# Optimization experiments

Measured on AMD Instinct MI355X. Metric: run time of the kernel, lower is better.

## Reference

```python
import jax, jax.numpy as jnp
import numpy as np

B = 2048
U_DIM = 128
N_USER = 500000
N_NEWS = 50000
N_WORD = 279215
TITLE_LEN = 10
W_EMB = 50
U_NB = 30   # user_neighbor
N_NB = 30   # news_neighbor
NCAPS = 8
NHID = 16
DIM = NCAPS * NHID          # 128
CNN_OUT = 128
ROUTIT = 4
CONV_CH, KH, KW = 8, 2, 20
PH, PW = 2, 1
FLAT = CONV_CH * ((TITLE_LEN - KH + 1) // PH) * (W_EMB - KW + 1)  # 8*4*31 = 992


def setup_inputs() -> dict:
    key = jax.random.key(0)
    ks = jax.random.split(key, 18)
    nrm = lambda k, s: jax.random.normal(k, s, jnp.float32) * 0.1
    return {
        "user_indices": jax.random.randint(ks[0], (B,), 0, N_USER),
        "news_indices": jax.random.randint(ks[1], (B,), 0, N_NEWS),
        "labels": (jax.random.uniform(ks[2], (B,)) > 0.5).astype(jnp.float32),
        # int neighbor / title tables (module buffers)
        "news_user": jax.random.randint(ks[3], (N_NEWS + 1, U_NB), 0, N_USER),
        "user_news": jax.random.randint(ks[4], (N_USER + 1, N_NB), 0, N_NEWS),
        "title": jax.random.randint(ks[5], (N_NEWS + 1, TITLE_LEN), 0, N_WORD),
        # float parameters
        "user_emb_matrix": nrm(ks[6], (N_USER + 1, U_DIM)),
        "word_emb_matrix": nrm(ks[7], (N_WORD + 1, W_EMB)),
        "conv_w": nrm(ks[8], (CONV_CH, 1, KH, KW)),
        "conv_b": jnp.zeros((CONV_CH,), jnp.float32),
        "dense_w": nrm(ks[9], (FLAT, CNN_OUT)),
        "dense_b": jnp.zeros((CNN_OUT,), jnp.float32),
        "user_weights": nrm(ks[10], (U_DIM, DIM)),
        "user_bias": nrm(ks[11], (DIM,)),
        "item_weights": nrm(ks[12], (CNN_OUT, DIM)),
        "item_bias": nrm(ks[13], (DIM,)),
        "last_w": nrm(ks[14], (DIM, DIM)),
        "last_b": jnp.zeros((DIM,), jnp.float32),
    }


def _convolution(news_ids, title, word_emb, conv_w, conv_b, dense_w, dense_b):
    """Title-CNN news encoder. news_ids: [B, K] int -> [B*K, CNN_OUT]."""
    bk = news_ids.shape[0] * news_ids.shape[1]
    words = title[news_ids.reshape(-1)]              # [BK, L] gather
    x = word_emb[words][:, None, :, :]               # [BK, 1, L, 50]
    y = jax.lax.conv_general_dilated(
        x, conv_w, (1, 1), 'VALID', dimension_numbers=('NCHW', 'OIHW', 'NCHW'))
    y = jax.nn.relu(y + conv_b[None, :, None, None])
    y = jax.lax.reduce_window(y, -jnp.inf, jax.lax.max,
                              (1, 1, PH, PW), (1, 1, PH, PW), 'VALID')
    return jax.nn.relu(y.reshape(bk, -1) @ dense_w + dense_b)


def _routing(x_self, z_nb):
    """Capsule neighbor routing. x_self: [B, DIM], z_nb: [B, K, DIM]."""
    l2n = lambda v: v / (jnp.linalg.norm(v, axis=-1, keepdims=True) + 1e-9)
    x = l2n(x_self.reshape(-1, NCAPS, NHID))
    z = l2n(z_nb.reshape(z_nb.shape[0], z_nb.shape[1], NCAPS, NHID))
    u = x
    for _ in range(ROUTIT):
        p = jax.nn.softmax(jnp.einsum('bkcd,bcd->bkc', z, u), axis=-1)  # over caps
        u = l2n(x + jnp.einsum('bkc,bkcd->bcd', p, z))
    return u.reshape(-1, DIM)


def reference(user_indices, news_indices, labels, news_user, user_news, title,
              user_emb_matrix, word_emb_matrix, conv_w, conv_b, dense_w, dense_b,
              user_weights, user_bias, item_weights, item_bias, last_w, last_b):
    # hop-0 (seed) vectors
    news_v0 = jax.nn.relu(
        _convolution(news_indices[:, None], title, word_emb_matrix,
                     conv_w, conv_b, dense_w, dense_b) @ item_weights + item_bias)  # [B, DIM]
    user_v0 = jax.nn.relu(user_emb_matrix[user_indices] @ user_weights + user_bias)  # [B, DIM]
    # hop-1 neighbor gathers
    news_nb = news_user[news_indices]   # [B, U_NB] user ids clicked this news
    user_nb = user_news[user_indices]   # [B, N_NB] news ids clicked by user
    news_v1 = jax.nn.relu(user_emb_matrix[news_nb] @ user_weights + user_bias)  # [B, U_NB, DIM]
    user_v1 = jax.nn.relu(
        _convolution(user_nb, title, word_emb_matrix, conv_w, conv_b,
                     dense_w, dense_b) @ item_weights + item_bias
    ).reshape(B, N_NB, DIM)
    # capsule routing aggregation
    news_emb = _routing(news_v0, news_v1)
    user_emb = _routing(user_v0, user_v1)
    # simple_dot_net scoring
    x_map = user_emb @ last_w + last_b
    y_map = news_emb @ last_w + last_b
    scores = jnp.sum(x_map * y_map, axis=-1)
    return jax.nn.sigmoid(scores)
```

## Files before the change

kernel.cpp:

```cpp
#include <hip/hip_runtime.h>
#include <hip/hip_bf16.h>
#include <math.h>

#define BSZ 2048
#define NNEWS 50000
#define U_NB 30
#define N_NB 30
#define TITLE_LEN 10
#define W_EMB 50
#define DIM 128
#define ROUTIT 4
#define FLAT2 1024
#define NJOBS (BSZ * 31)

typedef __attribute__((ext_vector_type(8))) short bf16x8;
typedef __attribute__((ext_vector_type(4))) float f32x4;

__device__ __forceinline__ ushort bfbits(float v) {
  __hip_bfloat16 h = __float2bfloat16(v);
  ushort u;
  __builtin_memcpy(&u, &h, 2);
  return u;
}

__device__ __forceinline__ bf16x8 bfrag(const ushort* row, int s) {
  const char* p = reinterpret_cast<const char*>(row) + ((s * 2) & ~15);
  const uint4 lo = *reinterpret_cast<const uint4*>(p);
  const uint4 hi = *reinterpret_cast<const uint4*>(p + 16);
  const uint d0 = lo.x, d1 = lo.y, d2 = lo.z, d3 = lo.w;
  const uint d4 = hi.x, d5 = hi.y, d6 = hi.z, d7 = hi.w;
  const bool q2 = (s & 4) != 0;
  const uint e0 = q2 ? d2 : d0, e1 = q2 ? d3 : d1, e2 = q2 ? d4 : d2;
  const uint e3 = q2 ? d5 : d3, e4 = q2 ? d6 : d4, e5 = q2 ? d7 : d5;
  const bool q1 = (s & 2) != 0;
  const uint f0 = q1 ? e1 : e0, f1 = q1 ? e2 : e1, f2 = q1 ? e3 : e2;
  const uint f3 = q1 ? e4 : e3, f4 = q1 ? e5 : e4;
  const bool r1 = (s & 1) != 0;
  uint g[4];
  g[0] = r1 ? ((f0 >> 16) | (f1 << 16)) : f0;
  g[1] = r1 ? ((f1 >> 16) | (f2 << 16)) : f1;
  g[2] = r1 ? ((f2 >> 16) | (f3 << 16)) : f2;
  g[3] = r1 ? ((f3 >> 16) | (f4 << 16)) : f3;
  bf16x8 r;
  __builtin_memcpy(&r, g, 16);
  return r;
}

__global__ __launch_bounds__(256) void k_prep(
    const float* __restrict__ dw, const float* __restrict__ iw,
    const float* __restrict__ uw, __hip_bfloat16* __restrict__ dwt,
    __hip_bfloat16* __restrict__ iwt, __hip_bfloat16* __restrict__ uwt) {
  const int idx = blockIdx.x * 256 + threadIdx.x;
  if (idx < DIM * FLAT2) {
    const int col = idx & 127, k2 = idx >> 7;
    const int i = k2 & 3, X = k2 >> 2;
    const int c = X & 7, gkq = (X >> 3) & 3, jhq = (X >> 5) & 1, h = X >> 6;
    const int j = jhq * 16 + gkq * 4 + i;
    const float v = (j < 31) ? dw[(c * 124 + h * 31 + j) * 128 + col] : 0.f;
    dwt[col * FLAT2 + k2] = __float2bfloat16(v);
  } else if (idx < DIM * FLAT2 + DIM * DIM) {
    const int j = idx - DIM * FLAT2;
    const int o = j & 127, k = j >> 7;
    iwt[o * DIM + k] = __float2bfloat16(iw[j]);
  } else if (idx < DIM * FLAT2 + 2 * DIM * DIM) {
    const int j = idx - DIM * FLAT2 - DIM * DIM;
    const int o = j & 127, k = j >> 7;
    uwt[o * DIM + k] = __float2bfloat16(uw[j]);
  }
}

__global__ __launch_bounds__(256, 4) void k_conv(
    const int* __restrict__ title, const float* __restrict__ word_emb,
    const float* __restrict__ conv_w, const float* __restrict__ conv_b,
    __hip_bfloat16* __restrict__ flat) {
  __shared__ int s_words[80];
  __shared__ __align__(16) ushort s_x[80 * 64];

  const int tid = threadIdx.x;
  const int wv = tid >> 6, lane = tid & 63;
  const int base = blockIdx.x * 8;
  const int c = lane & 15, gk = lane >> 4;

  bf16x8 b0, b1;
#pragma unroll
  for (int i = 0; i < 8; ++i) {
    const int k = gk * 8 + i;
    float v0 = 0.f, v1 = 0.f;
    if (c < 8 && k < 20) {
      v0 = conv_w[c * 40 + k];
      v1 = conv_w[c * 40 + 20 + k];
    }
    b0[i] = (short)bfbits(v0);
    b1[i] = (short)bfbits(v1);
  }
  const float cbias = (c < 8) ? conv_b[c] : 0.f;

  if (tid < 80) s_words[tid] = title[base * TITLE_LEN + tid];
  __syncthreads();

  {
    const float2* we2 = reinterpret_cast<const float2*>(word_emb);
#pragma unroll
    for (int i = 0; i < 3; ++i) {
      const int u = tid + i * 256;
      if (u < 640) {
        const int row = u >> 3, slot = u & 7;
        ushort o[8];
#pragma unroll
        for (int p = 0; p < 4; ++p) {
          const int c2 = slot * 4 + p;
          float2 v = make_float2(0.f, 0.f);
          if (c2 < 25) v = we2[(long long)s_words[row] * 25 + c2];
          o[2 * p] = bfbits(v.x);
          o[2 * p + 1] = bfbits(v.y);
        }
        *reinterpret_cast<uint4*>(&s_x[row * 64 + slot * 8]) =
            *reinterpret_cast<const uint4*>(o);
      }
    }
  }
  __syncthreads();

  ushort* fl = reinterpret_cast<ushort*>(flat);
#pragma unroll 1
  for (int tt = 0; tt < 2; ++tt) {
    const int t = wv * 2 + tt;
    const ushort* xb = &s_x[t * 640];
    ushort* gout = &fl[(size_t)(base + t) * FLAT2];
#pragma unroll
    for (int jh = 0; jh < 2; ++jh) {
      const int s = jh * 16 + (lane & 15) + gk * 8;
      bf16x8 fprev = bfrag(xb, s);
#pragma unroll
      for (int h = 0; h < 4; ++h) {
        const bf16x8 fmid = bfrag(xb + (2 * h + 1) * 64, s);
        const bf16x8 fnext = bfrag(xb + (2 * h + 2) * 64, s);
        f32x4 d0 = (f32x4){0.f, 0.f, 0.f, 0.f};
        f32x4 d1 = (f32x4){0.f, 0.f, 0.f, 0.f};
        d0 = __builtin_amdgcn_mfma_f32_16x16x32_bf16(fprev, b0, d0, 0, 0, 0);
        d0 = __builtin_amdgcn_mfma_f32_16x16x32_bf16(fmid, b1, d0, 0, 0, 0);
        d1 = __builtin_amdgcn_mfma_f32_16x16x32_bf16(fmid, b0, d1, 0, 0, 0);
        d1 = __builtin_amdgcn_mfma_f32_16x16x32_bf16(fnext, b1, d1, 0, 0, 0);
        if (c < 8) {
          ushort w[4];
#pragma unroll
          for (int i2 = 0; i2 < 4; ++i2)
            w[i2] = bfbits(fmaxf(fmaxf(d0[i2], d1[i2]) + cbias, 0.f));
          *reinterpret_cast<uint2*>(&gout[(h * 64 + jh * 32 + gk * 8 + c) * 4]) =
              *reinterpret_cast<const uint2*>(w);
        }
        fprev = fnext;
      }
    }
  }
}

__global__ __launch_bounds__(256, 2) void k_dense(
    const __hip_bfloat16* __restrict__ flat,
    const __hip_bfloat16* __restrict__ dwt, const float* __restrict__ dense_b,
    const __hip_bfloat16* __restrict__ iwt, const float* __restrict__ item_b,
    __hip_bfloat16* __restrict__ out, int nrows) {
  __shared__ __align__(16) char lds[18432];
  ushort* A0 = (ushort*)lds;
  ushort* A1 = (ushort*)(lds + 9216);
  ushort* c1 = (ushort*)lds;

  const int tid = threadIdx.x;
  const int wv = tid >> 6, lane = tid & 63;
  const int fr = lane & 15, gk = lane >> 4;
  const int lrow0 = min((int)blockIdx.x * 64, nrows - 64);
  const ushort* fl = (const ushort*)flat;
  const ushort* dwp = (const ushort*)dwt;

  uint4 pA[2];
#define LD_A(KS)                                                              \
  {                                                                           \
    _Pragma("unroll") for (int q = 0; q < 2; ++q) {                           \
      const int uu = tid + q * 256;                                           \
      pA[q] = *reinterpret_cast<const uint4*>(                                \
          &fl[(size_t)(lrow0 + (uu >> 3)) * FLAT2 + (KS) * 64 + (uu & 7) * 8]); \
    }                                                                         \
  }
#define ST_A(BUF)                                                             \
  {                                                                           \
    _Pragma("unroll") for (int q = 0; q < 2; ++q) {                           \
      const int uu = tid + q * 256;                                           \
      *reinterpret_cast<uint4*>(&(BUF)[(uu >> 3) * 72 + (uu & 7) * 8]) = pA[q]; \
    }                                                                         \
  }
#define LD_B(DST, KS)                                                         \
  {                                                                           \
    _Pragma("unroll") for (int nn = 0; nn < 2; ++nn)                          \
        _Pragma("unroll") for (int qq = 0; qq < 2; ++qq) {                    \
      (DST)[nn * 2 + qq] = *reinterpret_cast<const bf16x8*>(                  \
          &dwp[(wv * 32 + nn * 16 + fr) * FLAT2 + (KS) * 64 + qq * 32 +       \
               gk * 8]);                                                      \
    }                                                                         \
  }

  LD_A(0);
  ST_A(A0);
  LD_A(1);
  bf16x8 bA[4];
  LD_B(bA, 0);
  __syncthreads();

  f32x4 acc[4][2];
#pragma unroll
  for (int m = 0; m < 4; ++m)
#pragma unroll
    for (int n = 0; n < 2; ++n) acc[m][n] = (f32x4){0.f, 0.f, 0.f, 0.f};

  for (int ks = 0; ks < 16; ++ks) {
    const ushort* cA = (ks & 1) ? A1 : A0;
    bf16x8 bN[4];
    if (ks < 15) {
      LD_B(bN, ks + 1);
    } else {
#pragma unroll
      for (int z = 0; z < 4; ++z) bN[z] = bA[z];
    }
    bf16x8 af[2][4];
#pragma unroll
    for (int kk = 0; kk < 2; ++kk)
#pragma unroll
      for (int m = 0; m < 4; ++m)
        af[kk][m] = *reinterpret_cast<const bf16x8*>(
            &cA[(m * 16 + fr) * 72 + kk * 32 + gk * 8]);
#pragma unroll
    for (int kk = 0; kk < 2; ++kk)
#pragma unroll
      for (int m = 0; m < 4; ++m)
#pragma unroll
        for (int n = 0; n < 2; ++n)
          acc[m][n] = __builtin_amdgcn_mfma_f32_16x16x32_bf16(
              af[kk][m], bA[n * 2 + kk], acc[m][n], 0, 0, 0);
    if (ks < 15) {
      if (ks & 1) {
        ST_A(A0);
      } else {
        ST_A(A1);
      }
    }
    if (ks < 14) LD_A(ks + 2);
    __syncthreads();
#pragma unroll
    for (int z = 0; z < 4; ++z) bA[z] = bN[z];
  }
#undef LD_A
#undef ST_A
#undef LD_B

#pragma unroll
  for (int n = 0; n < 2; ++n) {
    const int col = wv * 32 + n * 16 + fr;
    const float bb = dense_b[col];
#pragma unroll
    for (int m = 0; m < 4; ++m)
#pragma unroll
      for (int r = 0; r < 4; ++r)
        c1[(m * 16 + gk * 4 + r) * 136 + col] =
            bfbits(fmaxf(acc[m][n][r] + bb, 0.f));
  }
  __syncthreads();

  const ushort* iwp = (const ushort*)iwt;
  f32x4 a2[4][2];
#pragma unroll
  for (int m = 0; m < 4; ++m)
#pragma unroll
    for (int n = 0; n < 2; ++n) a2[m][n] = (f32x4){0.f, 0.f, 0.f, 0.f};
#pragma unroll
  for (int kk = 0; kk < 4; ++kk) {
    bf16x8 af[4], bfr[2];
#pragma unroll
    for (int m = 0; m < 4; ++m)
      af[m] = *reinterpret_cast<const bf16x8*>(
          &c1[(m * 16 + fr) * 136 + kk * 32 + gk * 8]);
#pragma unroll
    for (int n = 0; n < 2; ++n)
      bfr[n] = *reinterpret_cast<const bf16x8*>(
          &iwp[(wv * 32 + n * 16 + fr) * DIM + kk * 32 + gk * 8]);
#pragma unroll
    for (int m = 0; m < 4; ++m)
#pragma unroll
      for (int n = 0; n < 2; ++n)
        a2[m][n] = __builtin_amdgcn_mfma_f32_16x16x32_bf16(af[m], bfr[n],
                                                           a2[m][n], 0, 0, 0);
  }

#pragma unroll
  for (int n = 0; n < 2; ++n) {
    const int col = wv * 32 + n * 16 + fr;
    const float bb = item_b[col];
#pragma unroll
    for (int m = 0; m < 4; ++m)
#pragma unroll
      for (int r = 0; r < 4; ++r) {
        const int row = m * 16 + gk * 4 + r;
        out[(size_t)(lrow0 + row) * DIM + col] =
            __float2bfloat16(fmaxf(a2[m][n][r] + bb, 0.f));
      }
  }
}

__global__ __launch_bounds__(256) void k_user(
    const int* __restrict__ user_indices, const int* __restrict__ news_indices,
    const int* __restrict__ news_user, const float* __restrict__ user_emb,
    const __hip_bfloat16* __restrict__ uwt, const float* __restrict__ user_b,
    __hip_bfloat16* __restrict__ out) {
  __shared__ __align__(16) __hip_bfloat16 s_e[32][136];
  __shared__ int s_uid[32];
  const int tid = threadIdx.x;
  const int wave = tid >> 6, lane = tid & 63;
  const int base = blockIdx.x * 32;

  if (tid < 32) {
    const int r = base + tid;
    int uid;
    if (r < BSZ) {
      uid = user_indices[r];
    } else {
      const int j = r - BSZ;
      const int b = j / U_NB, k = j - b * U_NB;
      uid = news_user[(long long)news_indices[b] * U_NB + k];
    }
    s_uid[tid] = uid;
  }
  __syncthreads();
#pragma unroll
  for (int i = 0; i < 4; ++i) {
    const int u = tid + i * 256;
    const int row = u >> 5, d4 = u & 31;
    const float4 v = *reinterpret_cast<const float4*>(
        &user_emb[(long long)s_uid[row] * DIM + d4 * 4]);
    __hip_bfloat16* p = &s_e[row][d4 * 4];
    p[0] = __float2bfloat16(v.x);
    p[1] = __float2bfloat16(v.y);
    p[2] = __float2bfloat16(v.z);
    p[3] = __float2bfloat16(v.w);
  }
  __syncthreads();

  const int fr = lane & 15, gk = lane >> 4;
  const ushort* uwp = (const ushort*)uwt;
  f32x4 acc[2][2];
#pragma unroll
  for (int m = 0; m < 2; ++m)
#pragma unroll
    for (int n = 0; n < 2; ++n) acc[m][n] = (f32x4){0.f, 0.f, 0.f, 0.f};

#pragma unroll
  for (int ks = 0; ks < 4; ++ks) {
    bf16x8 af[2], bfr[2];
#pragma unroll
    for (int m = 0; m < 2; ++m)
      af[m] = *reinterpret_cast<const bf16x8*>(
          &s_e[m * 16 + fr][ks * 32 + gk * 8]);
#pragma unroll
    for (int n = 0; n < 2; ++n)
      bfr[n] = *reinterpret_cast<const bf16x8*>(
          &uwp[(wave * 32 + n * 16 + fr) * DIM + ks * 32 + gk * 8]);
#pragma unroll
    for (int m = 0; m < 2; ++m)
#pragma unroll
      for (int n = 0; n < 2; ++n)
        acc[m][n] = __builtin_amdgcn_mfma_f32_16x16x32_bf16(af[m], bfr[n],
                                                            acc[m][n], 0, 0, 0);
  }

#pragma unroll
  for (int n = 0; n < 2; ++n) {
    const int col = wave * 32 + n * 16 + fr;
    const float bb = user_b[col];
#pragma unroll
    for (int m = 0; m < 2; ++m)
#pragma unroll
      for (int r = 0; r < 4; ++r) {
        const int row = m * 16 + gk * 4 + r;
        out[(size_t)(base + row) * DIM + col] =
            __float2bfloat16(fmaxf(acc[m][n][r] + bb, 0.f));
      }
  }
}

__device__ __forceinline__ float gsum16(float v) {
  v += __shfl_xor(v, 1, 16);
  v += __shfl_xor(v, 2, 16);
  v += __shfl_xor(v, 4, 16);
  v += __shfl_xor(v, 8, 16);
  return v;
}

__global__ __launch_bounds__(256) void k_route(
    const __hip_bfloat16* __restrict__ news_cnn,
    const __hip_bfloat16* __restrict__ user_path,
    const int* __restrict__ user_indices, const int* __restrict__ news_indices,
    const int* __restrict__ user_news, float* __restrict__ news_out,
    float* __restrict__ user_out) {
  __shared__ int s_nid[32];
  __shared__ __align__(16) float zf[30][132];
  __shared__ __align__(16) float xn[128];
  __shared__ __align__(16) float uu[128];
  __shared__ __align__(16) float pp[30][8];

  const int j = blockIdx.x, tid = threadIdx.x;
  const bool is_news = (j < BSZ);
  const int b = is_news ? j : j - BSZ;

  if (tid < 30)
    s_nid[tid] = is_news ? (BSZ + b * 30 + tid)
                         : user_news[(long long)user_indices[b] * N_NB + tid];
  __syncthreads();

  const __hip_bfloat16* zsrc = is_news ? user_path : news_cnn;
  if (tid < 240) {
    const int k = tid >> 3, q = tid & 7;
    const ushort* src =
        reinterpret_cast<const ushort*>(zsrc + (long long)s_nid[k] * DIM);
    ushort h16[16];
    *reinterpret_cast<uint4*>(&h16[0]) =
        *reinterpret_cast<const uint4*>(&src[q * 16]);
    *reinterpret_cast<uint4*>(&h16[8]) =
        *reinterpret_cast<const uint4*>(&src[q * 16 + 8]);
    float f[16];
#pragma unroll
    for (int i = 0; i < 16; ++i) {
      const uint bits = ((uint)h16[i]) << 16;
      __builtin_memcpy(&f[i], &bits, 4);
    }
#pragma unroll
    for (int v4 = 0; v4 < 4; ++v4)
      *reinterpret_cast<f32x4*>(&zf[k][q * 16 + v4 * 4]) =
          *reinterpret_cast<f32x4*>(&f[v4 * 4]);
  }
  if (tid < 128) {
    const __hip_bfloat16* xrow = is_news
                                     ? news_cnn + (long long)news_indices[b] * DIM
                                     : user_path + (long long)b * DIM;
    float xv = __bfloat162float(xrow[tid]);
    xv = xv / (sqrtf(gsum16(xv * xv)) + 1e-9f);
    xn[tid] = xv;
    uu[tid] = xv;
  }
  __syncthreads();

  const int kk = tid >> 3, cc = tid & 7;
  float z16[16];
  if (tid < 240) {
    float ss = 0.f;
#pragma unroll
    for (int d = 0; d < 16; ++d) {
      z16[d] = zf[kk][cc * 16 + d];
      ss += z16[d] * z16[d];
    }
    const float inv = 1.f / (sqrtf(ss) + 1e-9f);
#pragma unroll
    for (int d = 0; d < 16; ++d) {
      z16[d] *= inv;
      zf[kk][cc * 16 + d] = z16[d];
    }
  }
  __syncthreads();

  float u_fin = 0.f;
  for (int it = 0; it < ROUTIT; ++it) {
    if (tid < 240) {
      float dot = 0.f;
#pragma unroll
      for (int d = 0; d < 16; ++d) dot += z16[d] * uu[cc * 16 + d];
      pp[kk][cc] = dot;
    }
    __syncthreads();
    if (tid < 30) {
      float m = -1e30f, e[8], s = 0.f;
#pragma unroll
      for (int c2 = 0; c2 < 8; ++c2) m = fmaxf(m, pp[tid][c2]);
#pragma unroll
      for (int c2 = 0; c2 < 8; ++c2) {
        e[c2] = expf(pp[tid][c2] - m);
        s += e[c2];
      }
      const float invs = 1.f / s;
#pragma unroll
      for (int c2 = 0; c2 < 8; ++c2) pp[tid][c2] = e[c2] * invs;
    }
    __syncthreads();
    if (tid < 128) {
      const int c2 = tid >> 4;
      float agg = xn[tid];
#pragma unroll
      for (int k = 0; k < 30; ++k) agg += pp[k][c2] * zf[k][tid];
      u_fin = agg / (sqrtf(gsum16(agg * agg)) + 1e-9f);
      uu[tid] = u_fin;
    }
    __syncthreads();
  }
  if (tid < 128)
    (is_news ? news_out : user_out)[(long long)b * DIM + tid] = u_fin;
}

__global__ __launch_bounds__(128) void k_score(
    const float* __restrict__ user_e, const float* __restrict__ news_e,
    const float* __restrict__ last_w, const float* __restrict__ last_b,
    float* __restrict__ out) {
  const int b = blockIdx.x, tid = threadIdx.x;
  __shared__ float s_u[DIM], s_n[DIM];
  __shared__ float s_r[2];
  s_u[tid] = user_e[(long long)b * DIM + tid];
  s_n[tid] = news_e[(long long)b * DIM + tid];
  __syncthreads();
  float xm = last_b[tid], ym = last_b[tid];
  for (int k = 0; k < DIM; k += 4) {
#pragma unroll
    for (int i = 0; i < 4; ++i) {
      const float w = last_w[(k + i) * DIM + tid];
      xm += s_u[k + i] * w;
      ym += s_n[k + i] * w;
    }
  }
  float prod = xm * ym;
#pragma unroll
  for (int off = 1; off < 64; off <<= 1) prod += __shfl_xor(prod, off, 64);
  if ((tid & 63) == 0) s_r[tid >> 6] = prod;
  __syncthreads();
  if (tid == 0) {
    const float s = s_r[0] + s_r[1];
    out[b] = 1.f / (1.f + expf(-s));
  }
}

extern "C" void kernel_launch(void* const* d_in, const int* in_sizes, int n_in,
                              void* d_out, int out_size, void* d_ws,
                              size_t ws_size, hipStream_t stream) {
  (void)in_sizes; (void)n_in; (void)out_size; (void)ws_size;
  const int* user_indices = (const int*)d_in[0];
  const int* news_indices = (const int*)d_in[1];
  const int* news_user = (const int*)d_in[3];
  const int* user_news = (const int*)d_in[4];
  const int* title = (const int*)d_in[5];
  const float* user_emb_matrix = (const float*)d_in[6];
  const float* word_emb_matrix = (const float*)d_in[7];
  const float* conv_w = (const float*)d_in[8];
  const float* conv_b = (const float*)d_in[9];
  const float* dense_w = (const float*)d_in[10];
  const float* dense_b = (const float*)d_in[11];
  const float* user_weights = (const float*)d_in[12];
  const float* user_bias = (const float*)d_in[13];
  const float* item_weights = (const float*)d_in[14];
  const float* item_bias = (const float*)d_in[15];
  const float* last_w = (const float*)d_in[16];
  const float* last_b = (const float*)d_in[17];

  char* ws = (char*)d_ws;
  __hip_bfloat16* flat = (__hip_bfloat16*)ws;
  ws += (size_t)NNEWS * FLAT2 * 2;
  __hip_bfloat16* news_cnn = (__hip_bfloat16*)ws;
  ws += (size_t)NNEWS * DIM * 2;
  __hip_bfloat16* user_path = (__hip_bfloat16*)ws;
  ws += (size_t)NJOBS * DIM * 2;
  float* news_emb = (float*)ws;
  ws += (size_t)BSZ * DIM * 4;
  float* user_emb = (float*)ws;
  ws += (size_t)BSZ * DIM * 4;
  __hip_bfloat16* dwt = (__hip_bfloat16*)ws;
  ws += (size_t)DIM * FLAT2 * 2;
  __hip_bfloat16* iwt = (__hip_bfloat16*)ws;
  ws += (size_t)DIM * DIM * 2;
  __hip_bfloat16* uwt = (__hip_bfloat16*)ws;
  float* out = (float*)d_out;

  k_prep<<<(DIM * FLAT2 + 2 * DIM * DIM + 255) / 256, 256, 0, stream>>>(
      dense_w, item_weights, user_weights, dwt, iwt, uwt);
  k_conv<<<NNEWS / 8, 256, 0, stream>>>(title, word_emb_matrix, conv_w,
                                        conv_b, flat);
  k_dense<<<(NNEWS + 63) / 64, 256, 0, stream>>>(
      flat, dwt, dense_b, iwt, item_bias, news_cnn, NNEWS);
  k_user<<<NJOBS / 32, 256, 0, stream>>>(
      user_indices, news_indices, news_user, user_emb_matrix, uwt, user_bias,
      user_path);
  k_route<<<2 * BSZ, 256, 0, stream>>>(news_cnn, user_path, user_indices,
                                       news_indices, user_news, news_emb,
                                       user_emb);
  k_score<<<BSZ, 128, 0, stream>>>(user_emb, news_emb, last_w, last_b, out);
}
```

Measured before the change: 200.5 us.

## Encode only news titles referenced by the batch via a compacted id list

Previously the title CNN and dense layers ran over all news items. Two new kernels now mark which news ids are referenced by the batch (seed news and each user's clicked news) and compact them into a list with an atomic counter. k_conv and k_dense then process only the listed ids, exit early past the live count, and scatter results to each id's row in news_cnn. This removes encoder work for news the batch never reads, at the cost of a memset, two extra launches, a contended atomic counter, and rows written in a nondeterministic order.

```diff
diff --git a/kernel.cpp b/kernel.cpp
--- a/kernel.cpp
+++ b/kernel.cpp
@@ -46,6 +46,28 @@
   return r;
 }
 
+__global__ __launch_bounds__(256) void k_mark(
+    const int* __restrict__ news_indices, const int* __restrict__ user_indices,
+    const int* __restrict__ user_news, unsigned char* __restrict__ used) {
+  const int i = blockIdx.x * 256 + threadIdx.x;
+  if (i < BSZ) used[news_indices[i]] = 1;
+  const int j = i - BSZ;
+  if (j >= 0 && j < BSZ * N_NB) {
+    const int b = j / N_NB, k = j - b * N_NB;
+    used[user_news[(long long)user_indices[b] * N_NB + k]] = 1;
+  }
+}
+
+__global__ __launch_bounds__(256) void k_compact(
+    const unsigned char* __restrict__ used, int* __restrict__ list,
+    int* __restrict__ counter) {
+  const int id = blockIdx.x * 256 + threadIdx.x;
+  if (id < NNEWS && used[id]) {
+    const int p = atomicAdd(counter, 1);
+    list[p] = id;
+  }
+}
+
 __global__ __launch_bounds__(256) void k_prep(
     const float* __restrict__ dw, const float* __restrict__ iw,
     const float* __restrict__ uw, __hip_bfloat16* __restrict__ dwt,
@@ -72,13 +94,17 @@
 __global__ __launch_bounds__(256, 4) void k_conv(
     const int* __restrict__ title, const float* __restrict__ word_emb,
     const float* __restrict__ conv_w, const float* __restrict__ conv_b,
+    const int* __restrict__ list, const int* __restrict__ counter,
     __hip_bfloat16* __restrict__ flat) {
   __shared__ int s_words[80];
   __shared__ __align__(16) ushort s_x[80 * 64];
 
+  const int n = counter[0];
+  const int base = blockIdx.x * 8;
+  if (base >= n) return;
+
   const int tid = threadIdx.x;
   const int wv = tid >> 6, lane = tid & 63;
-  const int base = blockIdx.x * 8;
   const int c = lane & 15, gk = lane >> 4;
 
   bf16x8 b0, b1;
@@ -95,7 +121,11 @@
   }
   const float cbias = (c < 8) ? conv_b[c] : 0.f;
 
-  if (tid < 80) s_words[tid] = title[base * TITLE_LEN + tid];
+  if (tid < 80) {
+    const int idx = min(base + tid / 10, n - 1);
+    const int id = list[idx];
+    s_words[tid] = title[(long long)id * TITLE_LEN + (tid - (tid / 10) * 10)];
+  }
   __syncthreads();
 
   {
@@ -127,6 +157,7 @@
     const int t = wv * 2 + tt;
     const ushort* xb = &s_x[t * 640];
     ushort* gout = &fl[(size_t)(base + t) * FLAT2];
+    const bool live = (base + t) < n;
 #pragma unroll
     for (int jh = 0; jh < 2; ++jh) {
       const int s = jh * 16 + (lane & 15) + gk * 8;
@@ -141,7 +172,7 @@
         d0 = __builtin_amdgcn_mfma_f32_16x16x32_bf16(fmid, b1, d0, 0, 0, 0);
         d1 = __builtin_amdgcn_mfma_f32_16x16x32_bf16(fmid, b0, d1, 0, 0, 0);
         d1 = __builtin_amdgcn_mfma_f32_16x16x32_bf16(fnext, b1, d1, 0, 0, 0);
-        if (c < 8) {
+        if (c < 8 && live) {
           ushort w[4];
 #pragma unroll
           for (int i2 = 0; i2 < 4; ++i2)
@@ -159,16 +190,20 @@
     const __hip_bfloat16* __restrict__ flat,
     const __hip_bfloat16* __restrict__ dwt, const float* __restrict__ dense_b,
     const __hip_bfloat16* __restrict__ iwt, const float* __restrict__ item_b,
-    __hip_bfloat16* __restrict__ out, int nrows) {
+    const int* __restrict__ list, const int* __restrict__ counter,
+    __hip_bfloat16* __restrict__ out) {
   __shared__ __align__(16) char lds[18432];
   ushort* A0 = (ushort*)lds;
   ushort* A1 = (ushort*)(lds + 9216);
   ushort* c1 = (ushort*)lds;
 
+  const int n = counter[0];
+  const int lrow0 = (int)blockIdx.x * 64;
+  if (lrow0 >= n) return;
+
   const int tid = threadIdx.x;
   const int wv = tid >> 6, lane = tid & 63;
   const int fr = lane & 15, gk = lane >> 4;
-  const int lrow0 = min((int)blockIdx.x * 64, nrows - 64);
   const ushort* fl = (const ushort*)flat;
   const ushort* dwp = (const ushort*)dwt;
 
@@ -209,7 +244,7 @@
 #pragma unroll
   for (int m = 0; m < 4; ++m)
 #pragma unroll
-    for (int n = 0; n < 2; ++n) acc[m][n] = (f32x4){0.f, 0.f, 0.f, 0.f};
+    for (int n2 = 0; n2 < 2; ++n2) acc[m][n2] = (f32x4){0.f, 0.f, 0.f, 0.f};
 
   for (int ks = 0; ks < 16; ++ks) {
     const ushort* cA = (ks & 1) ? A1 : A0;
@@ -232,9 +267,9 @@
 #pragma unroll
       for (int m = 0; m < 4; ++m)
 #pragma unroll
-        for (int n = 0; n < 2; ++n)
-          acc[m][n] = __builtin_amdgcn_mfma_f32_16x16x32_bf16(
-              af[kk][m], bA[n * 2 + kk], acc[m][n], 0, 0, 0);
+        for (int n2 = 0; n2 < 2; ++n2)
+          acc[m][n2] = __builtin_amdgcn_mfma_f32_16x16x32_bf16(
+              af[kk][m], bA[n2 * 2 + kk], acc[m][n2], 0, 0, 0);
     if (ks < 15) {
       if (ks & 1) {
         ST_A(A0);
@@ -252,15 +287,15 @@
 #undef LD_B
 
 #pragma unroll
-  for (int n = 0; n < 2; ++n) {
-    const int col = wv * 32 + n * 16 + fr;
+  for (int n2 = 0; n2 < 2; ++n2) {
+    const int col = wv * 32 + n2 * 16 + fr;
     const float bb = dense_b[col];
 #pragma unroll
     for (int m = 0; m < 4; ++m)
 #pragma unroll
       for (int r = 0; r < 4; ++r)
         c1[(m * 16 + gk * 4 + r) * 136 + col] =
-            bfbits(fmaxf(acc[m][n][r] + bb, 0.f));
+            bfbits(fmaxf(acc[m][n2][r] + bb, 0.f));
   }
   __syncthreads();
 
@@ -269,7 +304,7 @@
 #pragma unroll
   for (int m = 0; m < 4; ++m)
 #pragma unroll
-    for (int n = 0; n < 2; ++n) a2[m][n] = (f32x4){0.f, 0.f, 0.f, 0.f};
+    for (int n2 = 0; n2 < 2; ++n2) a2[m][n2] = (f32x4){0.f, 0.f, 0.f, 0.f};
 #pragma unroll
   for (int kk = 0; kk < 4; ++kk) {
     bf16x8 af[4], bfr[2];
@@ -278,28 +313,32 @@
       af[m] = *reinterpret_cast<const bf16x8*>(
           &c1[(m * 16 + fr) * 136 + kk * 32 + gk * 8]);
 #pragma unroll
-    for (int n = 0; n < 2; ++n)
-      bfr[n] = *reinterpret_cast<const bf16x8*>(
-          &iwp[(wv * 32 + n * 16 + fr) * DIM + kk * 32 + gk * 8]);
+    for (int n2 = 0; n2 < 2; ++n2)
+      bfr[n2] = *reinterpret_cast<const bf16x8*>(
+          &iwp[(wv * 32 + n2 * 16 + fr) * DIM + kk * 32 + gk * 8]);
 #pragma unroll
     for (int m = 0; m < 4; ++m)
 #pragma unroll
-      for (int n = 0; n < 2; ++n)
-        a2[m][n] = __builtin_amdgcn_mfma_f32_16x16x32_bf16(af[m], bfr[n],
-                                                           a2[m][n], 0, 0, 0);
-  }
-
-#pragma unroll
-  for (int n = 0; n < 2; ++n) {
-    const int col = wv * 32 + n * 16 + fr;
+      for (int n2 = 0; n2 < 2; ++n2)
+        a2[m][n2] = __builtin_amdgcn_mfma_f32_16x16x32_bf16(af[m], bfr[n2],
+                                                            a2[m][n2], 0, 0, 0);
+  }
+
+#pragma unroll
+  for (int n2 = 0; n2 < 2; ++n2) {
+    const int col = wv * 32 + n2 * 16 + fr;
     const float bb = item_b[col];
 #pragma unroll
     for (int m = 0; m < 4; ++m)
 #pragma unroll
       for (int r = 0; r < 4; ++r) {
         const int row = m * 16 + gk * 4 + r;
-        out[(size_t)(lrow0 + row) * DIM + col] =
-            __float2bfloat16(fmaxf(a2[m][n][r] + bb, 0.f));
+        const int gr = lrow0 + row;
+        if (gr < n) {
+          const int id = list[gr];
+          out[(size_t)id * DIM + col] =
+              __float2bfloat16(fmaxf(a2[m][n2][r] + bb, 0.f));
+        }
       }
   }
 }
@@ -568,14 +607,25 @@
   __hip_bfloat16* iwt = (__hip_bfloat16*)ws;
   ws += (size_t)DIM * DIM * 2;
   __hip_bfloat16* uwt = (__hip_bfloat16*)ws;
+  ws += (size_t)DIM * DIM * 2;
+  unsigned char* used = (unsigned char*)ws;
+  ws += 50000;
+  int* counter = (int*)ws;
+  ws += 64;
+  int* list = (int*)ws;
   float* out = (float*)d_out;
 
+  hipMemsetAsync(used, 0, 50000 + 64, stream);
+
+  k_mark<<<(BSZ + BSZ * N_NB + 255) / 256, 256, 0, stream>>>(
+      news_indices, user_indices, user_news, used);
+  k_compact<<<(NNEWS + 255) / 256, 256, 0, stream>>>(used, list, counter);
   k_prep<<<(DIM * FLAT2 + 2 * DIM * DIM + 255) / 256, 256, 0, stream>>>(
       dense_w, item_weights, user_weights, dwt, iwt, uwt);
-  k_conv<<<NNEWS / 8, 256, 0, stream>>>(title, word_emb_matrix, conv_w,
-                                        conv_b, flat);
+  k_conv<<<(NNEWS + 7) / 8, 256, 0, stream>>>(
+      title, word_emb_matrix, conv_w, conv_b, list, counter, flat);
   k_dense<<<(NNEWS + 63) / 64, 256, 0, stream>>>(
-      flat, dwt, dense_b, iwt, item_bias, news_cnn, NNEWS);
+      flat, dwt, dense_b, iwt, item_bias, list, counter, news_cnn);
   k_user<<<NJOBS / 32, 256, 0, stream>>>(
       user_indices, news_indices, news_user, user_emb_matrix, uwt, user_bias,
       user_path);
```

Result: faster. 189.0 us (-5.7%).

## Merge six kernel launches into three by fusing independent and consecutive stages

Applied to the files above, without the earlier changes.

The weight-prep kernel becomes extra blocks of the conv kernel, and the news dense encoder and the user-embedding path now share one launch, split by block index. Routing for the news and user sides runs in one 512-thread block per batch item and scores directly, so the intermediate embedding buffers and the separate score kernel go away. This cuts launch overhead and global round-trips. The cost is heavier blocks and some occupancy risk from the larger shared-memory footprint in the back kernel.

```diff
diff --git a/kernel.cpp b/kernel.cpp
--- a/kernel.cpp
+++ b/kernel.cpp
@@ -12,6 +12,12 @@
 #define ROUTIT 4
 #define FLAT2 1024
 #define NJOBS (BSZ * 31)
+
+#define CONV_BLOCKS (NNEWS / 8)
+#define PREP_ELEMS (DIM * FLAT2 + 2 * DIM * DIM)
+#define PREP_BLOCKS (PREP_ELEMS / 256)
+#define DENSE_BLOCKS ((NNEWS + 63) / 64)
+#define USER_BLOCKS (NJOBS / 32)
 
 typedef __attribute__((ext_vector_type(8))) short bf16x8;
 typedef __attribute__((ext_vector_type(4))) float f32x4;
@@ -46,37 +52,39 @@
   return r;
 }
 
-__global__ __launch_bounds__(256) void k_prep(
-    const float* __restrict__ dw, const float* __restrict__ iw,
-    const float* __restrict__ uw, __hip_bfloat16* __restrict__ dwt,
-    __hip_bfloat16* __restrict__ iwt, __hip_bfloat16* __restrict__ uwt) {
-  const int idx = blockIdx.x * 256 + threadIdx.x;
-  if (idx < DIM * FLAT2) {
-    const int col = idx & 127, k2 = idx >> 7;
-    const int i = k2 & 3, X = k2 >> 2;
-    const int c = X & 7, gkq = (X >> 3) & 3, jhq = (X >> 5) & 1, h = X >> 6;
-    const int j = jhq * 16 + gkq * 4 + i;
-    const float v = (j < 31) ? dw[(c * 124 + h * 31 + j) * 128 + col] : 0.f;
-    dwt[col * FLAT2 + k2] = __float2bfloat16(v);
-  } else if (idx < DIM * FLAT2 + DIM * DIM) {
-    const int j = idx - DIM * FLAT2;
-    const int o = j & 127, k = j >> 7;
-    iwt[o * DIM + k] = __float2bfloat16(iw[j]);
-  } else if (idx < DIM * FLAT2 + 2 * DIM * DIM) {
-    const int j = idx - DIM * FLAT2 - DIM * DIM;
-    const int o = j & 127, k = j >> 7;
-    uwt[o * DIM + k] = __float2bfloat16(uw[j]);
-  }
-}
-
-__global__ __launch_bounds__(256, 4) void k_conv(
+__global__ __launch_bounds__(256, 4) void k_front(
     const int* __restrict__ title, const float* __restrict__ word_emb,
     const float* __restrict__ conv_w, const float* __restrict__ conv_b,
-    __hip_bfloat16* __restrict__ flat) {
+    const float* __restrict__ dw, const float* __restrict__ iw,
+    const float* __restrict__ uw, __hip_bfloat16* __restrict__ flat,
+    __hip_bfloat16* __restrict__ dwt, __hip_bfloat16* __restrict__ iwt,
+    __hip_bfloat16* __restrict__ uwt) {
+  const int tid = threadIdx.x;
+
+  if (blockIdx.x >= CONV_BLOCKS) {
+    const int idx = ((int)blockIdx.x - CONV_BLOCKS) * 256 + tid;
+    if (idx < DIM * FLAT2) {
+      const int col = idx & 127, k2 = idx >> 7;
+      const int i = k2 & 3, X = k2 >> 2;
+      const int c = X & 7, gkq = (X >> 3) & 3, jhq = (X >> 5) & 1, h = X >> 6;
+      const int j = jhq * 16 + gkq * 4 + i;
+      const float v = (j < 31) ? dw[(c * 124 + h * 31 + j) * 128 + col] : 0.f;
+      dwt[col * FLAT2 + k2] = __float2bfloat16(v);
+    } else if (idx < DIM * FLAT2 + DIM * DIM) {
+      const int j = idx - DIM * FLAT2;
+      const int o = j & 127, k = j >> 7;
+      iwt[o * DIM + k] = __float2bfloat16(iw[j]);
+    } else if (idx < PREP_ELEMS) {
+      const int j = idx - DIM * FLAT2 - DIM * DIM;
+      const int o = j & 127, k = j >> 7;
+      uwt[o * DIM + k] = __float2bfloat16(uw[j]);
+    }
+    return;
+  }
+
   __shared__ int s_words[80];
   __shared__ __align__(16) ushort s_x[80 * 64];
 
-  const int tid = threadIdx.x;
   const int wv = tid >> 6, lane = tid & 63;
   const int base = blockIdx.x * 8;
   const int c = lane & 15, gk = lane >> 4;
@@ -155,24 +163,30 @@
   }
 }
 
-__global__ __launch_bounds__(256, 2) void k_dense(
+__global__ __launch_bounds__(256, 2) void k_mid(
     const __hip_bfloat16* __restrict__ flat,
     const __hip_bfloat16* __restrict__ dwt, const float* __restrict__ dense_b,
     const __hip_bfloat16* __restrict__ iwt, const float* __restrict__ item_b,
-    __hip_bfloat16* __restrict__ out, int nrows) {
+    __hip_bfloat16* __restrict__ news_cnn,
+    const int* __restrict__ user_indices, const int* __restrict__ news_indices,
+    const int* __restrict__ news_user, const float* __restrict__ user_emb,
+    const __hip_bfloat16* __restrict__ uwt, const float* __restrict__ user_b,
+    __hip_bfloat16* __restrict__ user_path) {
   __shared__ __align__(16) char lds[18432];
-  ushort* A0 = (ushort*)lds;
-  ushort* A1 = (ushort*)(lds + 9216);
-  ushort* c1 = (ushort*)lds;
-
   const int tid = threadIdx.x;
   const int wv = tid >> 6, lane = tid & 63;
   const int fr = lane & 15, gk = lane >> 4;
-  const int lrow0 = min((int)blockIdx.x * 64, nrows - 64);
-  const ushort* fl = (const ushort*)flat;
-  const ushort* dwp = (const ushort*)dwt;
-
-  uint4 pA[2];
+
+  if (blockIdx.x < DENSE_BLOCKS) {
+    ushort* A0 = (ushort*)lds;
+    ushort* A1 = (ushort*)(lds + 9216);
+    ushort* c1 = (ushort*)lds;
+
+    const int lrow0 = min((int)blockIdx.x * 64, NNEWS - 64);
+    const ushort* fl = (const ushort*)flat;
+    const ushort* dwp = (const ushort*)dwt;
+
+    uint4 pA[2];
 #define LD_A(KS)                                                              \
   {                                                                           \
     _Pragma("unroll") for (int q = 0; q < 2; ++q) {                           \
@@ -198,122 +212,116 @@
     }                                                                         \
   }
 
-  LD_A(0);
-  ST_A(A0);
-  LD_A(1);
-  bf16x8 bA[4];
-  LD_B(bA, 0);
-  __syncthreads();
-
-  f32x4 acc[4][2];
-#pragma unroll
-  for (int m = 0; m < 4; ++m)
-#pragma unroll
-    for (int n = 0; n < 2; ++n) acc[m][n] = (f32x4){0.f, 0.f, 0.f, 0.f};
-
-  for (int ks = 0; ks < 16; ++ks) {
-    const ushort* cA = (ks & 1) ? A1 : A0;
-    bf16x8 bN[4];
-    if (ks < 15) {
-      LD_B(bN, ks + 1);
-    } else {
-#pragma unroll
-      for (int z = 0; z < 4; ++z) bN[z] = bA[z];
-    }
-    bf16x8 af[2][4];
-#pragma unroll
-    for (int kk = 0; kk < 2; ++kk)
-#pragma unroll
-      for (int m = 0; m < 4; ++m)
-        af[kk][m] = *reinterpret_cast<const bf16x8*>(
-            &cA[(m * 16 + fr) * 72 + kk * 32 + gk * 8]);
-#pragma unroll
-    for (int kk = 0; kk < 2; ++kk)
-#pragma unroll
-      for (int m = 0; m < 4; ++m)
-#pragma unroll
-        for (int n = 0; n < 2; ++n)
-          acc[m][n] = __builtin_amdgcn_mfma_f32_16x16x32_bf16(
-              af[kk][m], bA[n * 2 + kk], acc[m][n], 0, 0, 0);
-    if (ks < 15) {
-      if (ks & 1) {
-        ST_A(A0);
+    LD_A(0);
+    ST_A(A0);
+    LD_A(1);
+    bf16x8 bA[4];
+    LD_B(bA, 0);
+    __syncthreads();
+
+    f32x4 acc[4][2];
+#pragma unroll
+    for (int m = 0; m < 4; ++m)
+#pragma unroll
+      for (int n2 = 0; n2 < 2; ++n2) acc[m][n2] = (f32x4){0.f, 0.f, 0.f, 0.f};
+
+    for (int ks = 0; ks < 16; ++ks) {
+      const ushort* cA = (ks & 1) ? A1 : A0;
+      bf16x8 bN[4];
+      if (ks < 15) {
+        LD_B(bN, ks + 1);
       } else {
-        ST_A(A1);
-      }
-    }
-    if (ks < 14) LD_A(ks + 2);
-    __syncthreads();
-#pragma unroll
-    for (int z = 0; z < 4; ++z) bA[z] = bN[z];
-  }
+#pragma unroll
+        for (int z = 0; z < 4; ++z) bN[z] = bA[z];
+      }
+      bf16x8 af[2][4];
+#pragma unroll
+      for (int kk = 0; kk < 2; ++kk)
+#pragma unroll
+        for (int m = 0; m < 4; ++m)
+          af[kk][m] = *reinterpret_cast<const bf16x8*>(
+              &cA[(m * 16 + fr) * 72 + kk * 32 + gk * 8]);
+#pragma unroll
+      for (int kk = 0; kk < 2; ++kk)
+#pragma unroll
+        for (int m = 0; m < 4; ++m)
+#pragma unroll
+          for (int n2 = 0; n2 < 2; ++n2)
+            acc[m][n2] = __builtin_amdgcn_mfma_f32_16x16x32_bf16(
+                af[kk][m], bA[n2 * 2 + kk], acc[m][n2], 0, 0, 0);
+      if (ks < 15) {
+        if (ks & 1) {
+          ST_A(A0);
+        } else {
+          ST_A(A1);
+        }
+      }
+      if (ks < 14) LD_A(ks + 2);
+      __syncthreads();
+#pragma unroll
+      for (int z = 0; z < 4; ++z) bA[z] = bN[z];
+    }
 #undef LD_A
 #undef ST_A
 #undef LD_B
 
 #pragma unroll
-  for (int n = 0; n < 2; ++n) {
-    const int col = wv * 32 + n * 16 + fr;
-    const float bb = dense_b[col];
+    for (int n2 = 0; n2 < 2; ++n2) {
+      const int col = wv * 32 + n2 * 16 + fr;
+      const float bb = dense_b[col];
+#pragma unroll
+      for (int m = 0; m < 4; ++m)
+#pragma unroll
+        for (int r = 0; r < 4; ++r)
+          c1[(m * 16 + gk * 4 + r) * 136 + col] =
+              bfbits(fmaxf(acc[m][n2][r] + bb, 0.f));
+    }
+    __syncthreads();
+
+    const ushort* iwp = (const ushort*)iwt;
+    f32x4 a2[4][2];
 #pragma unroll
     for (int m = 0; m < 4; ++m)
 #pragma unroll
-      for (int r = 0; r < 4; ++r)
-        c1[(m * 16 + gk * 4 + r) * 136 + col] =
-            bfbits(fmaxf(acc[m][n][r] + bb, 0.f));
-  }
-  __syncthreads();
-
-  const ushort* iwp = (const ushort*)iwt;
-  f32x4 a2[4][2];
-#pragma unroll
-  for (int m = 0; m < 4; ++m)
-#pragma unroll
-    for (int n = 0; n < 2; ++n) a2[m][n] = (f32x4){0.f, 0.f, 0.f, 0.f};
-#pragma unroll
-  for (int kk = 0; kk < 4; ++kk) {
-    bf16x8 af[4], bfr[2];
-#pragma unroll
-    for (int m = 0; m < 4; ++m)
-      af[m] = *reinterpret_cast<const bf16x8*>(
-          &c1[(m * 16 + fr) * 136 + kk * 32 + gk * 8]);
-#pragma unroll
-    for (int n = 0; n < 2; ++n)
-      bfr[n] = *reinterpret_cast<const bf16x8*>(
-          &iwp[(wv * 32 + n * 16 + fr) * DIM + kk * 32 + gk * 8]);
-#pragma unroll
-    for (int m = 0; m < 4; ++m)
-#pragma unroll
-      for (int n = 0; n < 2; ++n)
-        a2[m][n] = __builtin_amdgcn_mfma_f32_16x16x32_bf16(af[m], bfr[n],
-                                                           a2[m][n], 0, 0, 0);
-  }
-
-#pragma unroll
-  for (int n = 0; n < 2; ++n) {
-    const int col = wv * 32 + n * 16 + fr;
-    const float bb = item_b[col];
-#pragma unroll
-    for (int m = 0; m < 4; ++m)
-#pragma unroll
-      for (int r = 0; r < 4; ++r) {
-        const int row = m * 16 + gk * 4 + r;
-        out[(size_t)(lrow0 + row) * DIM + col] =
-            __float2bfloat16(fmaxf(a2[m][n][r] + bb, 0.f));
-      }
-  }
-}
-
-__global__ __launch_bounds__(256) void k_user(
-    const int* __restrict__ user_indices, const int* __restrict__ news_indices,
-    const int* __restrict__ news_user, const float* __restrict__ user_emb,
-    const __hip_bfloat16* __restrict__ uwt, const float* __restrict__ user_b,
-    __hip_bfloat16* __restrict__ out) {
-  __shared__ __align__(16) __hip_bfloat16 s_e[32][136];
-  __shared__ int s_uid[32];
-  const int tid = threadIdx.x;
-  const int wave = tid >> 6, lane = tid & 63;
-  const int base = blockIdx.x * 32;
+      for (int n2 = 0; n2 < 2; ++n2) a2[m][n2] = (f32x4){0.f, 0.f, 0.f, 0.f};
+#pragma unroll
+    for (int kk = 0; kk < 4; ++kk) {
+      bf16x8 af[4], bfr[2];
+#pragma unroll
+      for (int m = 0; m < 4; ++m)
+        af[m] = *reinterpret_cast<const bf16x8*>(
+            &c1[(m * 16 + fr) * 136 + kk * 32 + gk * 8]);
+#pragma unroll
+      for (int n2 = 0; n2 < 2; ++n2)
+        bfr[n2] = *reinterpret_cast<const bf16x8*>(
+            &iwp[(wv * 32 + n2 * 16 + fr) * DIM + kk * 32 + gk * 8]);
+#pragma unroll
+      for (int m = 0; m < 4; ++m)
+#pragma unroll
+        for (int n2 = 0; n2 < 2; ++n2)
+          a2[m][n2] = __builtin_amdgcn_mfma_f32_16x16x32_bf16(
+              af[m], bfr[n2], a2[m][n2], 0, 0, 0);
+    }
+
+#pragma unroll
+    for (int n2 = 0; n2 < 2; ++n2) {
+      const int col = wv * 32 + n2 * 16 + fr;
+      const float bb = item_b[col];
+#pragma unroll
+      for (int m = 0; m < 4; ++m)
+#pragma unroll
+        for (int r = 0; r < 4; ++r) {
+          const int row = m * 16 + gk * 4 + r;
+          news_cnn[(size_t)(lrow0 + row) * DIM + col] =
+              __float2bfloat16(fmaxf(a2[m][n2][r] + bb, 0.f));
+        }
+    }
+    return;
+  }
+
+  __hip_bfloat16* s_e = (__hip_bfloat16*)lds;
+  int* s_uid = (int*)(lds + 8704);
+  const int base = ((int)blockIdx.x - DENSE_BLOCKS) * 32;
 
   if (tid < 32) {
     const int r = base + tid;
@@ -334,7 +342,7 @@
     const int row = u >> 5, d4 = u & 31;
     const float4 v = *reinterpret_cast<const float4*>(
         &user_emb[(long long)s_uid[row] * DIM + d4 * 4]);
-    __hip_bfloat16* p = &s_e[row][d4 * 4];
+    __hip_bfloat16* p = &s_e[row * 136 + d4 * 4];
     p[0] = __float2bfloat16(v.x);
     p[1] = __float2bfloat16(v.y);
     p[2] = __float2bfloat16(v.z);
@@ -342,7 +350,6 @@
   }
   __syncthreads();
 
-  const int fr = lane & 15, gk = lane >> 4;
   const ushort* uwp = (const ushort*)uwt;
   f32x4 acc[2][2];
 #pragma unroll
@@ -356,11 +363,11 @@
 #pragma unroll
     for (int m = 0; m < 2; ++m)
       af[m] = *reinterpret_cast<const bf16x8*>(
-          &s_e[m * 16 + fr][ks * 32 + gk * 8]);
+          &s_e[(m * 16 + fr) * 136 + ks * 32 + gk * 8]);
 #pragma unroll
     for (int n = 0; n < 2; ++n)
       bfr[n] = *reinterpret_cast<const bf16x8*>(
-          &uwp[(wave * 32 + n * 16 + fr) * DIM + ks * 32 + gk * 8]);
+          &uwp[(wv * 32 + n * 16 + fr) * DIM + ks * 32 + gk * 8]);
 #pragma unroll
     for (int m = 0; m < 2; ++m)
 #pragma unroll
@@ -371,14 +378,14 @@
 
 #pragma unroll
   for (int n = 0; n < 2; ++n) {
-    const int col = wave * 32 + n * 16 + fr;
+    const int col = wv * 32 + n * 16 + fr;
     const float bb = user_b[col];
 #pragma unroll
     for (int m = 0; m < 2; ++m)
 #pragma unroll
       for (int r = 0; r < 4; ++r) {
         const int row = m * 16 + gk * 4 + r;
-        out[(size_t)(base + row) * DIM + col] =
+        user_path[(size_t)(base + row) * DIM + col] =
             __float2bfloat16(fmaxf(acc[m][n][r] + bb, 0.f));
       }
   }
@@ -392,32 +399,38 @@
   return v;
 }
 
-__global__ __launch_bounds__(256) void k_route(
+__global__ __launch_bounds__(512) void k_back(
     const __hip_bfloat16* __restrict__ news_cnn,
     const __hip_bfloat16* __restrict__ user_path,
     const int* __restrict__ user_indices, const int* __restrict__ news_indices,
-    const int* __restrict__ user_news, float* __restrict__ news_out,
-    float* __restrict__ user_out) {
+    const int* __restrict__ user_news, const float* __restrict__ last_w,
+    const float* __restrict__ last_b, float* __restrict__ out) {
   __shared__ int s_nid[32];
-  __shared__ __align__(16) float zf[30][132];
-  __shared__ __align__(16) float xn[128];
-  __shared__ __align__(16) float uu[128];
-  __shared__ __align__(16) float pp[30][8];
-
-  const int j = blockIdx.x, tid = threadIdx.x;
-  const bool is_news = (j < BSZ);
-  const int b = is_news ? j : j - BSZ;
-
-  if (tid < 30)
-    s_nid[tid] = is_news ? (BSZ + b * 30 + tid)
-                         : user_news[(long long)user_indices[b] * N_NB + tid];
+  __shared__ __align__(16) float zf2[2][30][132];
+  __shared__ __align__(16) float xn2[2][128];
+  __shared__ __align__(16) float uu2[2][128];
+  __shared__ __align__(16) float pp2[2][30][8];
+  __shared__ float s_r[2];
+
+  const int b = blockIdx.x, tid = threadIdx.x;
+  const int hs = tid >> 8;
+  const int t = tid & 255;
+  const bool is_news = (hs == 0);
+  float(*zf)[132] = zf2[hs];
+  float* xn = xn2[hs];
+  float* uu = uu2[hs];
+  float(*pp)[8] = pp2[hs];
+
+  if (!is_news && t < 30)
+    s_nid[t] = user_news[(long long)user_indices[b] * N_NB + t];
   __syncthreads();
 
   const __hip_bfloat16* zsrc = is_news ? user_path : news_cnn;
-  if (tid < 240) {
-    const int k = tid >> 3, q = tid & 7;
+  if (t < 240) {
+    const int k = t >> 3, q = t & 7;
+    const int zid = is_news ? (BSZ + b * 30 + k) : s_nid[k];
     const ushort* src =
-        reinterpret_cast<const ushort*>(zsrc + (long long)s_nid[k] * DIM);
+        reinterpret_cast<const ushort*>(zsrc + (long long)zid * DIM);
     ushort h16[16];
     *reinterpret_cast<uint4*>(&h16[0]) =
         *reinterpret_cast<const uint4*>(&src[q * 16]);
@@ -434,20 +447,20 @@
       *reinterpret_cast<f32x4*>(&zf[k][q * 16 + v4 * 4]) =
           *reinterpret_cast<f32x4*>(&f[v4 * 4]);
   }
-  if (tid < 128) {
-    const __hip_bfloat16* xrow = is_news
-                                     ? news_cnn + (long long)news_indices[b] * DIM
-                                     : user_path + (long long)b * DIM;
-    float xv = __bfloat162float(xrow[tid]);
+  if (t < 128) {
+    const __hip_bfloat16* xrow =
+        is_news ? news_cnn + (long long)news_indices[b] * DIM
+                : user_path + (long long)b * DIM;
+    float xv = __bfloat162float(xrow[t]);
     xv = xv / (sqrtf(gsum16(xv * xv)) + 1e-9f);
-    xn[tid] = xv;
-    uu[tid] = xv;
-  }
-  __syncthreads();
-
-  const int kk = tid >> 3, cc = tid & 7;
+    xn[t] = xv;
+    uu[t] = xv;
+  }
+  __syncthreads();
+
+  const int kk = t >> 3, cc = t & 7;
   float z16[16];
-  if (tid < 240) {
+  if (t < 240) {
     float ss = 0.f;
 #pragma unroll
     for (int d = 0; d < 16; ++d) {
@@ -463,71 +476,55 @@
   }
   __syncthreads();
 
-  float u_fin = 0.f;
   for (int it = 0; it < ROUTIT; ++it) {
-    if (tid < 240) {
+    if (t < 240) {
       float dot = 0.f;
 #pragma unroll
       for (int d = 0; d < 16; ++d) dot += z16[d] * uu[cc * 16 + d];
       pp[kk][cc] = dot;
     }
     __syncthreads();
-    if (tid < 30) {
+    if (t < 30) {
       float m = -1e30f, e[8], s = 0.f;
 #pragma unroll
-      for (int c2 = 0; c2 < 8; ++c2) m = fmaxf(m, pp[tid][c2]);
+      for (int c2 = 0; c2 < 8; ++c2) m = fmaxf(m, pp[t][c2]);
 #pragma unroll
       for (int c2 = 0; c2 < 8; ++c2) {
-        e[c2] = expf(pp[tid][c2] - m);
+        e[c2] = expf(pp[t][c2] - m);
         s += e[c2];
       }
       const float invs = 1.f / s;
 #pragma unroll
-      for (int c2 = 0; c2 < 8; ++c2) pp[tid][c2] = e[c2] * invs;
+      for (int c2 = 0; c2 < 8; ++c2) pp[t][c2] = e[c2] * invs;
     }
     __syncthreads();
-    if (tid < 128) {
-      const int c2 = tid >> 4;
-      float agg = xn[tid];
-#pragma unroll
-      for (int k = 0; k < 30; ++k) agg += pp[k][c2] * zf[k][tid];
-      u_fin = agg / (sqrtf(gsum16(agg * agg)) + 1e-9f);
-      uu[tid] = u_fin;
+    if (t < 128) {
+      const int c2 = t >> 4;
+      float agg = xn[t];
+#pragma unroll
+      for (int k = 0; k < 30; ++k) agg += pp[k][c2] * zf[k][t];
+      uu[t] = agg / (sqrtf(gsum16(agg * agg)) + 1e-9f);
     }
     __syncthreads();
   }
-  if (tid < 128)
-    (is_news ? news_out : user_out)[(long long)b * DIM + tid] = u_fin;
-}
-
-__global__ __launch_bounds__(128) void k_score(
-    const float* __restrict__ user_e, const float* __restrict__ news_e,
-    const float* __restrict__ last_w, const float* __restrict__ last_b,
-    float* __restrict__ out) {
-  const int b = blockIdx.x, tid = threadIdx.x;
-  __shared__ float s_u[DIM], s_n[DIM];
-  __shared__ float s_r[2];
-  s_u[tid] = user_e[(long long)b * DIM + tid];
-  s_n[tid] = news_e[(long long)b * DIM + tid];
-  __syncthreads();
-  float xm = last_b[tid], ym = last_b[tid];
-  for (int k = 0; k < DIM; k += 4) {
-#pragma unroll
-    for (int i = 0; i < 4; ++i) {
-      const float w = last_w[(k + i) * DIM + tid];
-      xm += s_u[k + i] * w;
-      ym += s_n[k + i] * w;
-    }
-  }
-  float prod = xm * ym;
-#pragma unroll
-  for (int off = 1; off < 64; off <<= 1) prod += __shfl_xor(prod, off, 64);
-  if ((tid & 63) == 0) s_r[tid >> 6] = prod;
-  __syncthreads();
-  if (tid == 0) {
-    const float s = s_r[0] + s_r[1];
-    out[b] = 1.f / (1.f + expf(-s));
-  }
+
+  if (tid < 128) {
+    float xm = last_b[tid], ym = xm;
+    for (int k = 0; k < DIM; k += 4) {
+#pragma unroll
+      for (int i = 0; i < 4; ++i) {
+        const float w = last_w[(k + i) * DIM + tid];
+        xm += uu2[1][k + i] * w;
+        ym += uu2[0][k + i] * w;
+      }
+    }
+    float prod = xm * ym;
+#pragma unroll
+    for (int off = 1; off < 64; off <<= 1) prod += __shfl_xor(prod, off, 64);
+    if ((tid & 63) == 0) s_r[tid >> 6] = prod;
+  }
+  __syncthreads();
+  if (tid == 0) out[b] = 1.f / (1.f + expf(-(s_r[0] + s_r[1])));
 }
 
 extern "C" void kernel_launch(void* const* d_in, const int* in_sizes, int n_in,
@@ -559,10 +556,6 @@
   ws += (size_t)NNEWS * DIM * 2;
   __hip_bfloat16* user_path = (__hip_bfloat16*)ws;
   ws += (size_t)NJOBS * DIM * 2;
-  float* news_emb = (float*)ws;
-  ws += (size_t)BSZ * DIM * 4;
-  float* user_emb = (float*)ws;
-  ws += (size_t)BSZ * DIM * 4;
   __hip_bfloat16* dwt = (__hip_bfloat16*)ws;
   ws += (size_t)DIM * FLAT2 * 2;
   __hip_bfloat16* iwt = (__hip_bfloat16*)ws;
@@ -570,17 +563,13 @@
   __hip_bfloat16* uwt = (__hip_bfloat16*)ws;
   float* out = (float*)d_out;
 
-  k_prep<<<(DIM * FLAT2 + 2 * DIM * DIM + 255) / 256, 256, 0, stream>>>(
-      dense_w, item_weights, user_weights, dwt, iwt, uwt);
-  k_conv<<<NNEWS / 8, 256, 0, stream>>>(title, word_emb_matrix, conv_w,
-                                        conv_b, flat);
-  k_dense<<<(NNEWS + 63) / 64, 256, 0, stream>>>(
-      flat, dwt, dense_b, iwt, item_bias, news_cnn, NNEWS);
-  k_user<<<NJOBS / 32, 256, 0, stream>>>(
-      user_indices, news_indices, news_user, user_emb_matrix, uwt, user_bias,
-      user_path);
-  k_route<<<2 * BSZ, 256, 0, stream>>>(news_cnn, user_path, user_indices,
-                                       news_indices, user_news, news_emb,
-                                       user_emb);
-  k_score<<<BSZ, 128, 0, stream>>>(user_emb, news_emb, last_w, last_b, out);
-}
+  k_front<<<CONV_BLOCKS + PREP_BLOCKS, 256, 0, stream>>>(
+      title, word_emb_matrix, conv_w, conv_b, dense_w, item_weights,
+      user_weights, flat, dwt, iwt, uwt);
+  k_mid<<<DENSE_BLOCKS + USER_BLOCKS, 256, 0, stream>>>(
+      flat, dwt, dense_b, iwt, item_bias, news_cnn, user_indices, news_indices,
+      news_user, user_emb_matrix, uwt, user_bias, user_path);
+  k_back<<<BSZ, 512, 0, stream>>>(news_cnn, user_path, user_indices,
+                                  news_indices, user_news, last_w, last_b,
+                                  out);
+}
```

Measured after the change: 188.1 us. 6.2% less time.
